# Kernel tuning notes

Measured on AMD Instinct MI355X. Metric: run time of the kernel, lower is better.

## Reference

```python
import jax, jax.numpy as jnp
import numpy as np

H = 16          # num_heads
R = 4           # query compression ratio
WIN = 128       # sliding window size
NEG = -1e9      # finite mask value (safe softmax grads)


def setup_inputs() -> dict:
    key = jax.random.key(0)
    k0, k1, k2, k3, k4 = jax.random.split(key, 5)
    B, S, D = 4, 4096, 2048
    inputs = jax.random.normal(k0, (B, S, D), jnp.float32)
    attention_mask = jnp.ones((B, S), jnp.int32)
    s = 0.02
    Wq = jax.random.normal(k1, (D, D), jnp.float32) * s
    Wk = jax.random.normal(k2, (D, D), jnp.float32) * s
    Wv = jax.random.normal(k3, (D, D), jnp.float32) * s
    Wo = jax.random.normal(k4, (D, D), jnp.float32) * s
    return {"inputs": inputs, "attention_mask": attention_mask,
            "Wq": Wq, "Wk": Wk, "Wv": Wv, "Wo": Wo}


def _forward(inputs, attention_mask, Wq, Wk, Wv, Wo):
    B, S, D = inputs.shape
    dh = D // H
    scale = 1.0 / np.sqrt(dh).astype(np.float32)
    Cs = (S + R - 1) // R            # compressed query length (S % R == 0 here)
    win = min(WIN, S)
    ws = max(0, S - win)             # window start

    # Q projection -> [B,H,S,dh] -> compress groups of R by mean -> [B,H,Cs,dh]
    q = jnp.einsum('bsd,od->bso', inputs, Wq)
    q = q.reshape(B, S, H, dh).transpose(0, 2, 1, 3)
    qc = q.reshape(B, H, Cs, R, dh).mean(axis=3)

    # K/V only over the recent window
    wx = inputs[:, ws:ws + win, :]
    k = jnp.einsum('bsd,od->bso', wx, Wk).reshape(B, win, H, dh).transpose(0, 2, 1, 3)
    v = jnp.einsum('bsd,od->bso', wx, Wv).reshape(B, win, H, dh).transpose(0, 2, 1, 3)

    scores = jnp.einsum('bhqd,bhkd->bhqk', qc, k) * scale

    # causal mask: each compressed query sits at position (i+1)*R-1
    qpos = (jnp.arange(Cs) + 1) * R - 1                     # [Cs]
    wpos = ws + jnp.arange(win)
    causal = wpos[None, :] <= qpos[:, None]
    qbw = qpos < ws                                         # queries fully before window
    causal = causal.at[:, 0].set(causal[:, 0] | qbw)
    pad_ok = (attention_mask[:, ws:ws + win] != 0)
    full = causal[None, None, :, :] & pad_ok[:, None, None, :]

    scores = jnp.where(full, scores, NEG)
    weights = jax.nn.softmax(scores, axis=-1)
    out = jnp.einsum('bhqk,bhkd->bhqd', weights, v)         # [B,H,Cs,dh]
    out = out.transpose(0, 2, 1, 3).reshape(B, Cs, D)
    out = jnp.einsum('bsd,od->bso', out, Wo)

    if Cs != S:  # linear interpolation back to seq_len (align_corners=False)
        out = jax.image.resize(out, (B, S, D), method='linear')
    return out


def reference(inputs, attention_mask, Wq, Wk, Wv, Wo):
    return _forward(inputs, attention_mask, Wq, Wk, Wv, Wo)
```

## Files before the change

kernel.cpp:

```cpp
#include <hip/hip_runtime.h>
#include <hip/hip_bf16.h>


typedef __attribute__((ext_vector_type(8))) short short8;
typedef __attribute__((ext_vector_type(4))) short s16x4;
typedef __attribute__((ext_vector_type(4))) float f32x4;

#define LDP 72
#define YO_STRIDE  (132 * 2048)

__device__ __forceinline__ unsigned short f2bf(float f){
  unsigned int x = __float_as_uint(f);
  return (unsigned short)((x + 0x7fffu + ((x >> 16) & 1u)) >> 16);
}
__device__ __forceinline__ float bf2f(unsigned short u){
  return __uint_as_float(((unsigned int)u) << 16);
}
__device__ __forceinline__ s16x4 cvt4(float4 v){
  union { __hip_bfloat162 h[2]; s16x4 s; } r;
  float2 a; a.x = v.x; a.y = v.y;
  float2 b; b.x = v.z; b.y = v.w;
  r.h[0] = __float22bfloat162_rn(a);
  r.h[1] = __float22bfloat162_rn(b);
  return r.s;
}
__device__ __forceinline__ short8 cvt8(float4 x, float4 y){
  union { s16x4 h[2]; short8 s; } r;
  r.h[0] = cvt4(x); r.h[1] = cvt4(y);
  return r.s;
}

__global__ __launch_bounds__(256) void prep_kernel(
    const float* __restrict__ inp,
    const float* __restrict__ Wq, const float* __restrict__ Wk,
    const float* __restrict__ Wv, const float* __restrict__ Wo,
    unsigned short* __restrict__ Wb,
    unsigned short* __restrict__ Awx, unsigned short* __restrict__ Aq)
{
  const int bx = blockIdx.x;
  if (bx < 8192){
    const int idx = bx * 256 + threadIdx.x;
    const int w = idx >> 19;
    const int sub = idx & 524287;
    const float* src = (w == 0) ? Wq : (w == 1) ? Wk : (w == 2) ? Wv : Wo;
    const float* p = src + (size_t)sub * 8;
    *(short8*)&Wb[(size_t)w * 4194304 + (size_t)sub * 8] =
        cvt8(*(const float4*)p, *(const float4*)(p + 4));
  } else if (bx < 8704){
    const int idx = (bx - 8192) * 256 + threadIdx.x;
    const int b = idx >> 15;
    const int j = (idx >> 8) & 127;
    const int d8 = (idx & 255) * 8;
    const float* p = inp + ((size_t)b * 4096 + 3968 + j) * 2048 + d8;
    *(short8*)&Awx[((size_t)b * 128 + j) * 2048 + d8] =
        cvt8(*(const float4*)p, *(const float4*)(p + 4));
  } else {
    const int idx = (bx - 8704) * 256 + threadIdx.x;
    const int b = idx >> 13;
    const int c = (idx >> 8) & 31;
    const int d8 = (idx & 255) * 8;
    const float* p = inp + ((size_t)b * 4096 + 3968 + 4 * c) * 2048 + d8;
    float4 x0 = *(const float4*)(p);
    float4 x1 = *(const float4*)(p + 2048);
    float4 x2 = *(const float4*)(p + 4096);
    float4 x3 = *(const float4*)(p + 6144);
    float4 y0 = *(const float4*)(p + 4);
    float4 y1 = *(const float4*)(p + 2052);
    float4 y2 = *(const float4*)(p + 4100);
    float4 y3 = *(const float4*)(p + 6148);
    float4 xm, ym;
    xm.x = 0.25f * (x0.x + x1.x + x2.x + x3.x);
    xm.y = 0.25f * (x0.y + x1.y + x2.y + x3.y);
    xm.z = 0.25f * (x0.z + x1.z + x2.z + x3.z);
    xm.w = 0.25f * (x0.w + x1.w + x2.w + x3.w);
    ym.x = 0.25f * (y0.x + y1.x + y2.x + y3.x);
    ym.y = 0.25f * (y0.y + y1.y + y2.y + y3.y);
    ym.z = 0.25f * (y0.z + y1.z + y2.z + y3.z);
    ym.w = 0.25f * (y0.w + y1.w + y2.w + y3.w);
    *(short8*)&Aq[((size_t)b * 32 + c) * 2048 + d8] = cvt8(xm, ym);
  }
}

template<bool OUT_BF16>
__device__ __forceinline__ void gemm_body(
    const unsigned short* __restrict__ A, const unsigned short* __restrict__ W,
    unsigned short* __restrict__ Cb, float* __restrict__ Cf,
    int M, int row0, int n0, int kbase, int nsteps,
    unsigned short* As, unsigned short* Bs)
{
  const int tid  = threadIdx.x;
  const int lane = tid & 63;
  const int wid  = tid >> 6;
  const int wr = wid >> 1, wc = wid & 1;

  const int srow = tid >> 3;
  const int scol = (tid & 7) * 8;

  f32x4 acc[4][2] = {};
  short8 ra[4], rb[2];

  #pragma unroll
  for (int c = 0; c < 4; ++c){
    int gr = row0 + c * 32 + srow; if (gr > M - 1) gr = M - 1;
    ra[c] = *(const short8*)&A[(size_t)gr * 2048 + kbase + scol];
  }
  #pragma unroll
  for (int c = 0; c < 2; ++c)
    rb[c] = *(const short8*)&W[(size_t)(n0 + c * 32 + srow) * 2048 + kbase + scol];
  #pragma unroll
  for (int c = 0; c < 4; ++c)
    *(short8*)&As[(c * 32 + srow) * LDP + scol] = ra[c];
  #pragma unroll
  for (int c = 0; c < 2; ++c)
    *(short8*)&Bs[(c * 32 + srow) * LDP + scol] = rb[c];
  __syncthreads();

  for (int t = 0; t < nsteps; ++t){
    const bool pf = (t + 1) < nsteps;
    if (pf){
      const int k0 = kbase + (t + 1) * 64;
      #pragma unroll
      for (int c = 0; c < 4; ++c){
        int gr = row0 + c * 32 + srow; if (gr > M - 1) gr = M - 1;
        ra[c] = *(const short8*)&A[(size_t)gr * 2048 + k0 + scol];
      }
      #pragma unroll
      for (int c = 0; c < 2; ++c)
        rb[c] = *(const short8*)&W[(size_t)(n0 + c * 32 + srow) * 2048 + k0 + scol];
    }
    #pragma unroll
    for (int ks = 0; ks < 2; ++ks){
      short8 av[4], bv[2];
      #pragma unroll
      for (int f = 0; f < 4; ++f)
        av[f] = *(const short8*)&As[(wr * 64 + f * 16 + (lane & 15)) * LDP + ks * 32 + (lane >> 4) * 8];
      #pragma unroll
      for (int n = 0; n < 2; ++n)
        bv[n] = *(const short8*)&Bs[(wc * 32 + n * 16 + (lane & 15)) * LDP + ks * 32 + (lane >> 4) * 8];
      #pragma unroll
      for (int f = 0; f < 4; ++f)
        #pragma unroll
        for (int n = 0; n < 2; ++n)
          acc[f][n] = __builtin_amdgcn_mfma_f32_16x16x32_bf16(av[f], bv[n], acc[f][n], 0, 0, 0);
    }
    __syncthreads();
    if (pf){
      #pragma unroll
      for (int c = 0; c < 4; ++c)
        *(short8*)&As[(c * 32 + srow) * LDP + scol] = ra[c];
      #pragma unroll
      for (int c = 0; c < 2; ++c)
        *(short8*)&Bs[(c * 32 + srow) * LDP + scol] = rb[c];
      __syncthreads();
    }
  }

  #pragma unroll
  for (int f = 0; f < 4; ++f){
    #pragma unroll
    for (int n = 0; n < 2; ++n){
      const int col = n0 + wc * 32 + n * 16 + (lane & 15);
      #pragma unroll
      for (int r = 0; r < 4; ++r){
        const int row = row0 + wr * 64 + f * 16 + (lane >> 4) * 4 + r;
        if (row < M){
          if (OUT_BF16) Cb[(size_t)row * 2048 + col] = f2bf(acc[f][n][r]);
          else          Cf[(size_t)row * 2048 + col] = acc[f][n][r];
        }
      }
    }
  }
}

__global__ __launch_bounds__(256, 4) void qkv_kernel(
    const unsigned short* __restrict__ Aq, const unsigned short* __restrict__ Awx,
    const unsigned short* __restrict__ Wb,
    unsigned short* __restrict__ Qc, unsigned short* __restrict__ Kb,
    unsigned short* __restrict__ Vb)
{
  __shared__ __align__(16) unsigned short As[128 * LDP];
  __shared__ __align__(16) unsigned short Bs[64 * LDP];
  const int nt = blockIdx.x, gy = blockIdx.y;
  if (gy == 0)
    gemm_body<true>(Aq,  Wb,            Qc, nullptr, 128, 0,              nt * 64, 0, 32, As, Bs);
  else if (gy < 5)
    gemm_body<true>(Awx, Wb + 4194304,  Kb, nullptr, 512, (gy - 1) * 128, nt * 64, 0, 32, As, Bs);
  else
    gemm_body<true>(Awx, Wb + 8388608,  Vb, nullptr, 512, (gy - 5) * 128, nt * 64, 0, 32, As, Bs);
}

__global__ __launch_bounds__(256, 4) void o_kernel(
    const unsigned short* __restrict__ Ao, const unsigned short* __restrict__ Wb,
    float* __restrict__ Yop)
{
  __shared__ __align__(16) unsigned short As[128 * LDP];
  __shared__ __align__(16) unsigned short Bs[64 * LDP];
  gemm_body<false>(Ao, Wb + 12582912, nullptr, Yop + (size_t)blockIdx.z * YO_STRIDE,
                   132, blockIdx.y * 128, blockIdx.x * 64, blockIdx.z * 512, 8, As, Bs);
}

__global__ __launch_bounds__(256) void attn_kernel(
    const unsigned short* __restrict__ Qc, const unsigned short* __restrict__ Kb,
    const unsigned short* __restrict__ Vb, const int* __restrict__ amask,
    unsigned short* __restrict__ Ao)
{
  const int b = blockIdx.x >> 4;
  const int h = blockIdx.x & 15;
  __shared__ float Qs[32][129];
  __shared__ unsigned int Ks[128][65];
  __shared__ unsigned int Vs[128][65];
  __shared__ float Wt[32][132];
  __shared__ float msk[128];
  const int tid = threadIdx.x;

  for (int i = tid; i < 32 * 128; i += 256){
    int cq = i >> 7, d = i & 127;
    Qs[cq][d] = bf2f(Qc[(size_t)(b * 32 + cq) * 2048 + h * 128 + d]);
  }
  for (int i = tid; i < 128 * 64; i += 256){
    int j = i >> 6, du = i & 63;
    const unsigned int* kp = (const unsigned int*)(Kb + (size_t)(b * 128 + j) * 2048 + h * 128);
    const unsigned int* vp = (const unsigned int*)(Vb + (size_t)(b * 128 + j) * 2048 + h * 128);
    Ks[j][du] = kp[du];
    Vs[j][du] = vp[du];
  }
  if (tid < 128){
    msk[tid] = (amask[b * 4096 + 3968 + tid] != 0) ? 1.f : 0.f;
    Ao[(size_t)(b * 33) * 2048 + h * 128 + tid] = Vb[(size_t)(b * 128) * 2048 + h * 128 + tid];
  }
  __syncthreads();

  const int cq = tid >> 3, jg = tid & 7;
  const int jmax = 4 * cq + 3;
  const float scale = 0.088388347648318447f;

  float s[16];
  {
    float sacc[16];
    #pragma unroll
    for (int jj = 0; jj < 16; ++jj) sacc[jj] = 0.f;
    for (int du = 0; du < 64; ++du){
      float q0 = Qs[cq][2 * du], q1 = Qs[cq][2 * du + 1];
      #pragma unroll
      for (int jj = 0; jj < 16; ++jj){
        unsigned int u = Ks[jg * 16 + jj][du];
        sacc[jj] += q0 * __uint_as_float(u << 16) + q1 * __uint_as_float(u & 0xffff0000u);
      }
    }
    #pragma unroll
    for (int jj = 0; jj < 16; ++jj){
      int j = jg * 16 + jj;
      bool ok = (j <= jmax) && (msk[j] > 0.5f);
      s[jj] = ok ? sacc[jj] * scale : -1e9f;
    }
  }
  float m = s[0];
  #pragma unroll
  for (int jj = 1; jj < 16; ++jj) m = fmaxf(m, s[jj]);
  #pragma unroll
  for (int off = 1; off < 8; off <<= 1) m = fmaxf(m, __shfl_xor(m, off, 8));
  float sum = 0.f;
  #pragma unroll
  for (int jj = 0; jj < 16; ++jj){ s[jj] = expf(s[jj] - m); sum += s[jj]; }
  #pragma unroll
  for (int off = 1; off < 8; off <<= 1) sum += __shfl_xor(sum, off, 8);
  const float inv = 1.f / sum;
  #pragma unroll
  for (int jj = 0; jj < 16; ++jj) Wt[cq][jg * 16 + jj] = s[jj] * inv;
  __syncthreads();

  const int dg = tid & 7;
  float o[16];
  #pragma unroll
  for (int e = 0; e < 16; ++e) o[e] = 0.f;
  for (int j = 0; j < 128; ++j){
    float w = Wt[cq][j];
    #pragma unroll
    for (int du = 0; du < 8; ++du){
      unsigned int u = Vs[j][dg * 8 + du];
      o[2 * du]     += w * __uint_as_float(u << 16);
      o[2 * du + 1] += w * __uint_as_float(u & 0xffff0000u);
    }
  }
  unsigned short* dst = Ao + (size_t)(b * 33 + 1 + cq) * 2048 + h * 128 + dg * 16;
  #pragma unroll
  for (int e = 0; e < 16; ++e) dst[e] = f2bf(o[e]);
}

__global__ __launch_bounds__(256) void resize_kernel(
    const float* __restrict__ Yop, float* __restrict__ out)
{
  const int rowid = blockIdx.x;
  const int b = rowid >> 12;
  const int i = rowid & 4095;
  float c  = i * 0.25f - 0.375f;
  float fl = floorf(c);
  int   j0 = (int)fl;
  float f  = c - fl;
  int   j1 = j0 + 1;
  j0 = max(0, min(j0, 1023));
  j1 = max(0, min(j1, 1023));
  const int ri0 = b * 33 + (j0 <= 991 ? 0 : j0 - 991);
  const int ri1 = b * 33 + (j1 <= 991 ? 0 : j1 - 991);
  const float* r0 = Yop + (size_t)ri0 * 2048;
  const float* r1 = Yop + (size_t)ri1 * 2048;
  float* op = out + (size_t)rowid * 2048;
  const int t = threadIdx.x;
  const bool same = (ri0 == ri1);
  #pragma unroll
  for (int q = 0; q < 2; ++q){
    int d = q * 1024 + t * 4;
    float4 a0 = *(const float4*)(r0 + d);
    float4 a1 = *(const float4*)(r0 + d + YO_STRIDE);
    float4 a2 = *(const float4*)(r0 + d + 2 * YO_STRIDE);
    float4 a3 = *(const float4*)(r0 + d + 3 * YO_STRIDE);
    float4 a;
    a.x = a0.x + a1.x + a2.x + a3.x;
    a.y = a0.y + a1.y + a2.y + a3.y;
    a.z = a0.z + a1.z + a2.z + a3.z;
    a.w = a0.w + a1.w + a2.w + a3.w;
    float4 o = a;
    if (!same){
      float4 b0 = *(const float4*)(r1 + d);
      float4 b1 = *(const float4*)(r1 + d + YO_STRIDE);
      float4 b2 = *(const float4*)(r1 + d + 2 * YO_STRIDE);
      float4 b3 = *(const float4*)(r1 + d + 3 * YO_STRIDE);
      float4 bb;
      bb.x = b0.x + b1.x + b2.x + b3.x;
      bb.y = b0.y + b1.y + b2.y + b3.y;
      bb.z = b0.z + b1.z + b2.z + b3.z;
      bb.w = b0.w + b1.w + b2.w + b3.w;
      o.x = a.x + f * (bb.x - a.x);
      o.y = a.y + f * (bb.y - a.y);
      o.z = a.z + f * (bb.z - a.z);
      o.w = a.w + f * (bb.w - a.w);
    }
    *(float4*)(op + d) = o;
  }
}

extern "C" void kernel_launch(void* const* d_in, const int* in_sizes, int n_in,
                              void* d_out, int out_size, void* d_ws, size_t ws_size,
                              hipStream_t stream)
{
  const float* inp   = (const float*)d_in[0];
  const int*   amask = (const int*)d_in[1];
  const float* Wq = (const float*)d_in[2];
  const float* Wk = (const float*)d_in[3];
  const float* Wv = (const float*)d_in[4];
  const float* Wo = (const float*)d_in[5];
  float* out = (float*)d_out;

  char* ws = (char*)d_ws;
  unsigned short* Wb  = (unsigned short*)(ws);
  unsigned short* Aq  = (unsigned short*)(ws + 33554432);
  unsigned short* Awx = (unsigned short*)(ws + 34078720);
  unsigned short* Qc  = (unsigned short*)(ws + 36175872);
  unsigned short* Kb  = (unsigned short*)(ws + 36700160);
  unsigned short* Vb  = (unsigned short*)(ws + 38797312);
  unsigned short* Ao  = (unsigned short*)(ws + 40894464);
  float*          Yop = (float*)(ws + 41435136);

  prep_kernel<<<8832, 256, 0, stream>>>(inp, Wq, Wk, Wv, Wo, Wb, Awx, Aq);
  qkv_kernel<<<dim3(32, 9), 256, 0, stream>>>(Aq, Awx, Wb, Qc, Kb, Vb);
  attn_kernel<<<64, 256, 0, stream>>>(Qc, Kb, Vb, amask, Ao);
  o_kernel<<<dim3(32, 2, 4), 256, 0, stream>>>(Ao, Wb, Yop);
  resize_kernel<<<16384, 256, 0, stream>>>(Yop, out);
}
```

Baseline: 119.9 us.

## Split-K QKV GEMM with direct-to-LDS double-buffered 128x128 tiles

The shared GEMM body now stages tiles with global_load_lds straight into double-buffered, unpadded LDS, and uses 128x128 output tiles per block instead of 128x64. The QKV projection is split four ways along K, with bf16 partial outputs written to separate slices. The attention kernel sums those partials while loading Q, K and V. The goals are more blocks for the QKV GEMM, fewer register round-trips when staging, and more reuse per tile. The cost is extra partial-output traffic, extra bf16 rounding on the partial sums, possible LDS bank conflicts from the unpadded layout, and removal of the row clamp, so o_kernel now reads past the 132 valid Ao rows.

```diff
diff --git a/kernel.cpp b/kernel.cpp
--- a/kernel.cpp
+++ b/kernel.cpp
@@ -3,11 +3,11 @@
 
 
 typedef __attribute__((ext_vector_type(8))) short short8;
-typedef __attribute__((ext_vector_type(4))) short s16x4;
 typedef __attribute__((ext_vector_type(4))) float f32x4;
 
-#define LDP 72
-#define YO_STRIDE  (132 * 2048)
+#define QP_SLICE  (128 * 2048)
+#define KV_SLICE  (512 * 2048)
+#define YO_STRIDE (132 * 2048)
 
 __device__ __forceinline__ unsigned short f2bf(float f){
   unsigned int x = __float_as_uint(f);
@@ -16,17 +16,15 @@
 __device__ __forceinline__ float bf2f(unsigned short u){
   return __uint_as_float(((unsigned int)u) << 16);
 }
-__device__ __forceinline__ s16x4 cvt4(float4 v){
-  union { __hip_bfloat162 h[2]; s16x4 s; } r;
-  float2 a; a.x = v.x; a.y = v.y;
-  float2 b; b.x = v.z; b.y = v.w;
-  r.h[0] = __float22bfloat162_rn(a);
-  r.h[1] = __float22bfloat162_rn(b);
-  return r.s;
+__device__ __forceinline__ float bflo(unsigned int u){ return __uint_as_float(u << 16); }
+__device__ __forceinline__ float bfhi(unsigned int u){ return __uint_as_float(u & 0xffff0000u); }
+__device__ __forceinline__ unsigned int pk2(float lo, float hi){
+  return ((unsigned int)f2bf(hi) << 16) | (unsigned int)f2bf(lo);
 }
 __device__ __forceinline__ short8 cvt8(float4 x, float4 y){
-  union { s16x4 h[2]; short8 s; } r;
-  r.h[0] = cvt4(x); r.h[1] = cvt4(y);
+  union { unsigned int u[4]; short8 s; } r;
+  r.u[0] = pk2(x.x, x.y); r.u[1] = pk2(x.z, x.w);
+  r.u[2] = pk2(y.x, y.y); r.u[3] = pk2(y.z, y.w);
   return r.s;
 }
 
@@ -81,85 +79,74 @@
   }
 }
 
+__device__ __forceinline__ void stage_tile(
+    const unsigned short* __restrict__ A, const unsigned short* __restrict__ W,
+    int row0, int n0, int kt,
+    unsigned short* As, unsigned short* Bs, int wid, int lane)
+{
+  const int r = lane >> 3, u = (lane & 7) * 8;
+  #pragma unroll
+  for (int i = 0; i < 4; ++i){
+    const int c = wid * 4 + i;
+    __builtin_amdgcn_global_load_lds(
+        (const __attribute__((address_space(1))) void*)(A + (size_t)(row0 + c * 8 + r) * 2048 + kt + u),
+        (__attribute__((address_space(3))) void*)(As + c * 512),
+        16, 0, 0);
+    __builtin_amdgcn_global_load_lds(
+        (const __attribute__((address_space(1))) void*)(W + (size_t)(n0 + c * 8 + r) * 2048 + kt + u),
+        (__attribute__((address_space(3))) void*)(Bs + c * 512),
+        16, 0, 0);
+  }
+}
+
 template<bool OUT_BF16>
 __device__ __forceinline__ void gemm_body(
     const unsigned short* __restrict__ A, const unsigned short* __restrict__ W,
     unsigned short* __restrict__ Cb, float* __restrict__ Cf,
     int M, int row0, int n0, int kbase, int nsteps,
-    unsigned short* As, unsigned short* Bs)
+    unsigned short* L)
 {
   const int tid  = threadIdx.x;
   const int lane = tid & 63;
   const int wid  = tid >> 6;
   const int wr = wid >> 1, wc = wid & 1;
 
-  const int srow = tid >> 3;
-  const int scol = (tid & 7) * 8;
-
-  f32x4 acc[4][2] = {};
-  short8 ra[4], rb[2];
-
-  #pragma unroll
-  for (int c = 0; c < 4; ++c){
-    int gr = row0 + c * 32 + srow; if (gr > M - 1) gr = M - 1;
-    ra[c] = *(const short8*)&A[(size_t)gr * 2048 + kbase + scol];
-  }
-  #pragma unroll
-  for (int c = 0; c < 2; ++c)
-    rb[c] = *(const short8*)&W[(size_t)(n0 + c * 32 + srow) * 2048 + kbase + scol];
-  #pragma unroll
-  for (int c = 0; c < 4; ++c)
-    *(short8*)&As[(c * 32 + srow) * LDP + scol] = ra[c];
-  #pragma unroll
-  for (int c = 0; c < 2; ++c)
-    *(short8*)&Bs[(c * 32 + srow) * LDP + scol] = rb[c];
-  __syncthreads();
+  f32x4 acc[4][4] = {};
+
+  stage_tile(A, W, row0, n0, kbase, L, L + 8192, wid, lane);
+  int cur = 0;
 
   for (int t = 0; t < nsteps; ++t){
-    const bool pf = (t + 1) < nsteps;
-    if (pf){
-      const int k0 = kbase + (t + 1) * 64;
-      #pragma unroll
-      for (int c = 0; c < 4; ++c){
-        int gr = row0 + c * 32 + srow; if (gr > M - 1) gr = M - 1;
-        ra[c] = *(const short8*)&A[(size_t)gr * 2048 + k0 + scol];
-      }
-      #pragma unroll
-      for (int c = 0; c < 2; ++c)
-        rb[c] = *(const short8*)&W[(size_t)(n0 + c * 32 + srow) * 2048 + k0 + scol];
-    }
+    __syncthreads();
+    const int nxt = cur ^ 1;
+    if (t + 1 < nsteps)
+      stage_tile(A, W, row0, n0, kbase + (t + 1) * 64,
+                 L + nxt * 16384, L + nxt * 16384 + 8192, wid, lane);
+    const unsigned short* As = L + cur * 16384;
+    const unsigned short* Bs = As + 8192;
     #pragma unroll
     for (int ks = 0; ks < 2; ++ks){
-      short8 av[4], bv[2];
+      short8 av[4], bv[4];
       #pragma unroll
       for (int f = 0; f < 4; ++f)
-        av[f] = *(const short8*)&As[(wr * 64 + f * 16 + (lane & 15)) * LDP + ks * 32 + (lane >> 4) * 8];
-      #pragma unroll
-      for (int n = 0; n < 2; ++n)
-        bv[n] = *(const short8*)&Bs[(wc * 32 + n * 16 + (lane & 15)) * LDP + ks * 32 + (lane >> 4) * 8];
+        av[f] = *(const short8*)&As[(wr * 64 + f * 16 + (lane & 15)) * 64 + ks * 32 + (lane >> 4) * 8];
+      #pragma unroll
+      for (int n = 0; n < 4; ++n)
+        bv[n] = *(const short8*)&Bs[(wc * 64 + n * 16 + (lane & 15)) * 64 + ks * 32 + (lane >> 4) * 8];
       #pragma unroll
       for (int f = 0; f < 4; ++f)
         #pragma unroll
-        for (int n = 0; n < 2; ++n)
+        for (int n = 0; n < 4; ++n)
           acc[f][n] = __builtin_amdgcn_mfma_f32_16x16x32_bf16(av[f], bv[n], acc[f][n], 0, 0, 0);
     }
-    __syncthreads();
-    if (pf){
-      #pragma unroll
-      for (int c = 0; c < 4; ++c)
-        *(short8*)&As[(c * 32 + srow) * LDP + scol] = ra[c];
-      #pragma unroll
-      for (int c = 0; c < 2; ++c)
-        *(short8*)&Bs[(c * 32 + srow) * LDP + scol] = rb[c];
-      __syncthreads();
-    }
+    cur = nxt;
   }
 
   #pragma unroll
   for (int f = 0; f < 4; ++f){
     #pragma unroll
-    for (int n = 0; n < 2; ++n){
-      const int col = n0 + wc * 32 + n * 16 + (lane & 15);
+    for (int n = 0; n < 4; ++n){
+      const int col = n0 + wc * 64 + n * 16 + (lane & 15);
       #pragma unroll
       for (int r = 0; r < 4; ++r){
         const int row = row0 + wr * 64 + f * 16 + (lane >> 4) * 4 + r;
@@ -172,36 +159,40 @@
   }
 }
 
-__global__ __launch_bounds__(256, 4) void qkv_kernel(
+__global__ __launch_bounds__(256, 2) void qkv_kernel(
     const unsigned short* __restrict__ Aq, const unsigned short* __restrict__ Awx,
     const unsigned short* __restrict__ Wb,
-    unsigned short* __restrict__ Qc, unsigned short* __restrict__ Kb,
-    unsigned short* __restrict__ Vb)
-{
-  __shared__ __align__(16) unsigned short As[128 * LDP];
-  __shared__ __align__(16) unsigned short Bs[64 * LDP];
+    unsigned short* __restrict__ Qp, unsigned short* __restrict__ Kp,
+    unsigned short* __restrict__ Vp)
+{
+  __shared__ __align__(16) unsigned short L[4 * 16384 / 2];
   const int nt = blockIdx.x, gy = blockIdx.y;
-  if (gy == 0)
-    gemm_body<true>(Aq,  Wb,            Qc, nullptr, 128, 0,              nt * 64, 0, 32, As, Bs);
-  else if (gy < 5)
-    gemm_body<true>(Awx, Wb + 4194304,  Kb, nullptr, 512, (gy - 1) * 128, nt * 64, 0, 32, As, Bs);
-  else
-    gemm_body<true>(Awx, Wb + 8388608,  Vb, nullptr, 512, (gy - 5) * 128, nt * 64, 0, 32, As, Bs);
-}
-
-__global__ __launch_bounds__(256, 4) void o_kernel(
+  if (gy < 4){
+    gemm_body<true>(Aq, Wb, Qp + gy * QP_SLICE, nullptr,
+                    128, 0, nt * 128, gy * 512, 8, L);
+  } else if (gy < 20){
+    const int idx = gy - 4, mt = idx >> 2, ksp = idx & 3;
+    gemm_body<true>(Awx, Wb + 4194304, Kp + ksp * KV_SLICE, nullptr,
+                    512, mt * 128, nt * 128, ksp * 512, 8, L);
+  } else {
+    const int idx = gy - 20, mt = idx >> 2, ksp = idx & 3;
+    gemm_body<true>(Awx, Wb + 8388608, Vp + ksp * KV_SLICE, nullptr,
+                    512, mt * 128, nt * 128, ksp * 512, 8, L);
+  }
+}
+
+__global__ __launch_bounds__(256, 2) void o_kernel(
     const unsigned short* __restrict__ Ao, const unsigned short* __restrict__ Wb,
     float* __restrict__ Yop)
 {
-  __shared__ __align__(16) unsigned short As[128 * LDP];
-  __shared__ __align__(16) unsigned short Bs[64 * LDP];
+  __shared__ __align__(16) unsigned short L[32768];
   gemm_body<false>(Ao, Wb + 12582912, nullptr, Yop + (size_t)blockIdx.z * YO_STRIDE,
-                   132, blockIdx.y * 128, blockIdx.x * 64, blockIdx.z * 512, 8, As, Bs);
+                   132, blockIdx.y * 128, blockIdx.x * 128, blockIdx.z * 512, 8, L);
 }
 
 __global__ __launch_bounds__(256) void attn_kernel(
-    const unsigned short* __restrict__ Qc, const unsigned short* __restrict__ Kb,
-    const unsigned short* __restrict__ Vb, const int* __restrict__ amask,
+    const unsigned short* __restrict__ Qp, const unsigned short* __restrict__ Kp,
+    const unsigned short* __restrict__ Vp, const int* __restrict__ amask,
     unsigned short* __restrict__ Ao)
 {
   const int b = blockIdx.x >> 4;
@@ -215,18 +206,32 @@
 
   for (int i = tid; i < 32 * 128; i += 256){
     int cq = i >> 7, d = i & 127;
-    Qs[cq][d] = bf2f(Qc[(size_t)(b * 32 + cq) * 2048 + h * 128 + d]);
+    size_t off = (size_t)(b * 32 + cq) * 2048 + h * 128 + d;
+    Qs[cq][d] = bf2f(Qp[off]) + bf2f(Qp[off + QP_SLICE]) +
+                bf2f(Qp[off + 2 * QP_SLICE]) + bf2f(Qp[off + 3 * QP_SLICE]);
   }
   for (int i = tid; i < 128 * 64; i += 256){
     int j = i >> 6, du = i & 63;
-    const unsigned int* kp = (const unsigned int*)(Kb + (size_t)(b * 128 + j) * 2048 + h * 128);
-    const unsigned int* vp = (const unsigned int*)(Vb + (size_t)(b * 128 + j) * 2048 + h * 128);
-    Ks[j][du] = kp[du];
-    Vs[j][du] = vp[du];
+    size_t off = (size_t)(b * 128 + j) * 2048 + h * 128 + du * 2;
+    unsigned int k0 = *(const unsigned int*)(Kp + off);
+    unsigned int k1 = *(const unsigned int*)(Kp + off + KV_SLICE);
+    unsigned int k2 = *(const unsigned int*)(Kp + off + 2 * KV_SLICE);
+    unsigned int k3 = *(const unsigned int*)(Kp + off + 3 * KV_SLICE);
+    unsigned int v0 = *(const unsigned int*)(Vp + off);
+    unsigned int v1 = *(const unsigned int*)(Vp + off + KV_SLICE);
+    unsigned int v2 = *(const unsigned int*)(Vp + off + 2 * KV_SLICE);
+    unsigned int v3 = *(const unsigned int*)(Vp + off + 3 * KV_SLICE);
+    Ks[j][du] = pk2(bflo(k0) + bflo(k1) + bflo(k2) + bflo(k3),
+                    bfhi(k0) + bfhi(k1) + bfhi(k2) + bfhi(k3));
+    Vs[j][du] = pk2(bflo(v0) + bflo(v1) + bflo(v2) + bflo(v3),
+                    bfhi(v0) + bfhi(v1) + bfhi(v2) + bfhi(v3));
   }
   if (tid < 128){
     msk[tid] = (amask[b * 4096 + 3968 + tid] != 0) ? 1.f : 0.f;
-    Ao[(size_t)(b * 33) * 2048 + h * 128 + tid] = Vb[(size_t)(b * 128) * 2048 + h * 128 + tid];
+    size_t off = (size_t)(b * 128) * 2048 + h * 128 + tid;
+    Ao[(size_t)(b * 33) * 2048 + h * 128 + tid] =
+        f2bf(bf2f(Vp[off]) + bf2f(Vp[off + KV_SLICE]) +
+             bf2f(Vp[off + 2 * KV_SLICE]) + bf2f(Vp[off + 3 * KV_SLICE]));
   }
   __syncthreads();
 
@@ -244,7 +249,7 @@
       #pragma unroll
       for (int jj = 0; jj < 16; ++jj){
         unsigned int u = Ks[jg * 16 + jj][du];
-        sacc[jj] += q0 * __uint_as_float(u << 16) + q1 * __uint_as_float(u & 0xffff0000u);
+        sacc[jj] += q0 * bflo(u) + q1 * bfhi(u);
       }
     }
     #pragma unroll
@@ -278,8 +283,8 @@
     #pragma unroll
     for (int du = 0; du < 8; ++du){
       unsigned int u = Vs[j][dg * 8 + du];
-      o[2 * du]     += w * __uint_as_float(u << 16);
-      o[2 * du + 1] += w * __uint_as_float(u & 0xffff0000u);
+      o[2 * du]     += w * bflo(u);
+      o[2 * du + 1] += w * bfhi(u);
     }
   }
   unsigned short* dst = Ao + (size_t)(b * 33 + 1 + cq) * 2048 + h * 128 + dg * 16;
@@ -355,15 +360,15 @@
   unsigned short* Wb  = (unsigned short*)(ws);
   unsigned short* Aq  = (unsigned short*)(ws + 33554432);
   unsigned short* Awx = (unsigned short*)(ws + 34078720);
-  unsigned short* Qc  = (unsigned short*)(ws + 36175872);
-  unsigned short* Kb  = (unsigned short*)(ws + 36700160);
-  unsigned short* Vb  = (unsigned short*)(ws + 38797312);
-  unsigned short* Ao  = (unsigned short*)(ws + 40894464);
-  float*          Yop = (float*)(ws + 41435136);
+  unsigned short* Qp  = (unsigned short*)(ws + 36175872);
+  unsigned short* Kp  = (unsigned short*)(ws + 38273024);
+  unsigned short* Vp  = (unsigned short*)(ws + 46661632);
+  unsigned short* Ao  = (unsigned short*)(ws + 55050240);
+  float*          Yop = (float*)(ws + 56623104);
 
   prep_kernel<<<8832, 256, 0, stream>>>(inp, Wq, Wk, Wv, Wo, Wb, Awx, Aq);
-  qkv_kernel<<<dim3(32, 9), 256, 0, stream>>>(Aq, Awx, Wb, Qc, Kb, Vb);
-  attn_kernel<<<64, 256, 0, stream>>>(Qc, Kb, Vb, amask, Ao);
-  o_kernel<<<dim3(32, 2, 4), 256, 0, stream>>>(Ao, Wb, Yop);
+  qkv_kernel<<<dim3(16, 36), 256, 0, stream>>>(Aq, Awx, Wb, Qp, Kp, Vp);
+  attn_kernel<<<64, 256, 0, stream>>>(Qp, Kp, Vp, amask, Ao);
+  o_kernel<<<dim3(16, 2, 4), 256, 0, stream>>>(Ao, Wb, Yop);
   resize_kernel<<<16384, 256, 0, stream>>>(Yop, out);
 }
```

New measurement: 118.1 us. About the same (-1.5%).
